# Optimization experiments

Measured on AMD Instinct MI355X. Metric: run time of the kernel, lower is better.

## Reference

```python
import jax, jax.numpy as jnp
import numpy as np

B, C_IN, H, W = 4, 256, 56, 56
REL, OUT, SP, K, PAD = 16, 256, 8, 7, 3
WS = OUT // SP            # 32 attention-weight channels
K2 = K * K                # 49 window taps
EPS = 1e-5


def _unfold(x, k, pad):
    # reflect-pad (SAN pad_mode=1 -> *_refpad kernels) then gather kxk window taps
    # x: [B,C,H,W] -> [B,C,k*k,H,W], tap order row-major (matches torch Unfold)
    xp = jnp.pad(x, ((0, 0), (0, 0), (pad, pad), (pad, pad)), mode='reflect')
    h, w = x.shape[2], x.shape[3]
    return jnp.stack([xp[:, :, i:i + h, j:j + w]
                      for i in range(k) for j in range(k)], axis=2)


def _conv1x1(x, w, b):
    return jnp.einsum('bchw,oc->bohw', x, w) + b[None, :, None, None]


def _bn(x, g, b, m, v):
    # eval-mode BatchNorm2d over channel axis 1, broadcast over trailing dims
    shape = (1, -1) + (1,) * (x.ndim - 2)
    scale = g.reshape(shape) * jax.lax.rsqrt(v.reshape(shape) + EPS)
    return (x - m.reshape(shape)) * scale + b.reshape(shape)


def _forward(x, w1, b1, w2, b2, w3, b3,
             bn1_g, bn1_b, bn1_m, bn1_v, cw1_w,
             bn2_g, bn2_b, bn2_m, bn2_v, cw2_w, cw2_b, pos2_w):
    x1 = _conv1x1(x, w1, b1)          # [B,REL,H,W]  (query)
    x2 = _conv1x1(x, w2, b2)          # [B,REL,H,W]  (key)
    x3 = _conv1x1(x, w3, b3)          # [B,OUT,H,W]  (value)

    # Subtraction2: q_i - k_j for each of K2 window taps -> [B,REL,K2,H,W]
    diff = x1[:, :, None, :, :] - _unfold(x2, K, PAAD) if False else x1[:, :, None, :, :] - _unfold(x2, K, PAD)

    # conv_w: BN -> ReLU -> 1x1 (no bias) -> BN -> ReLU -> 1x1 (bias)
    h = jax.nn.relu(_bn(diff, bn1_g, bn1_b, bn1_m, bn1_v))
    h = jnp.einsum('bckhw,oc->bokhw', h, cw1_w)
    h = jax.nn.relu(_bn(h, bn2_g, bn2_b, bn2_m, bn2_v))
    h = jnp.einsum('bckhw,oc->bokhw', h, cw2_w) + cw2_b[None, :, None, None, None]
    w = jax.nn.softmax(h, axis=2)     # softmax over K2 taps -> [B,WS,K2,H,W]

    # Aggregation: out[b,c,p] = sum_k unfold(x3)[b,c,k,p] * w[b, c//SP, k, p]
    unf3 = _unfold(x3, K, PAD).reshape(B, WS, SP, K2, H, W)
    agg = jnp.einsum('bgskhw,bgkhw->bgshw', unf3, w).reshape(B, OUT, H, W)

    # use_position2: interleave aggregated values with w, grouped 1x1 conv
    xv = agg.reshape(B, SP, WS, H, W).transpose(0, 2, 1, 3, 4)   # [B,WS,SP,H,W]
    xc = jnp.concatenate([xv, w], axis=2)                        # [B,WS,SP+K2,H,W]
    out = jnp.einsum('bgihw,goi->bgohw', xc, pos2_w).reshape(B, OUT, H, W)
    return out


def setup_inputs() -> dict:
    key = jax.random.key(0)
    ks = jax.random.split(key, 20)
    n = lambda k, s, sc=1.0: jax.random.normal(k, s, dtype=jnp.float32) * sc
    u = lambda k, s: jax.random.uniform(k, s, dtype=jnp.float32, minval=0.5, maxval=1.5)
    return {
        'x': n(ks[0], (B, C_IN, H, W)),
        'w1': n(ks[1], (REL, C_IN), 0.05), 'b1': n(ks[2], (REL,), 0.05),
        'w2': n(ks[3], (REL, C_IN), 0.05), 'b2': n(ks[4], (REL,), 0.05),
        'w3': n(ks[5], (OUT, C_IN), 0.05), 'b3': n(ks[6], (OUT,), 0.05),
        'bn1_g': u(ks[7], (REL,)), 'bn1_b': n(ks[8], (REL,), 0.1),
        'bn1_m': n(ks[9], (REL,), 0.1), 'bn1_v': u(ks[10], (REL,)),
        'cw1_w': n(ks[11], (REL, REL), 0.2),
        'bn2_g': u(ks[12], (REL,)), 'bn2_b': n(ks[13], (REL,), 0.1),
        'bn2_m': n(ks[14], (REL,), 0.1), 'bn2_v': u(ks[15], (REL,)),
        'cw2_w': n(ks[16], (WS, REL), 0.2), 'cw2_b': n(ks[17], (WS,), 0.05),
        'pos2_w': n(ks[18], (WS, SP, SP + K2), 0.1),
    }


def reference(x, w1, b1, w2, b2, w3, b3,
              bn1_g, bn1_b, bn1_m, bn1_v, cw1_w,
              bn2_g, bn2_b, bn2_m, bn2_v, cw2_w, cw2_b, pos2_w):
    return _forward(x, w1, b1, w2, b2, w3, b3,
                    bn1_g, bn1_b, bn1_m, bn1_v, cw1_w,
                    bn2_g, bn2_b, bn2_m, bn2_v, cw2_w, cw2_b, pos2_w)
```

## Files before the change

### kernel.cpp

```cpp
#include <hip/hip_runtime.h>

#define HW 56
#define NPIX 3136
#define CIN 256
#define OUTC 256
#define LOG2E 1.4426950408889634f

typedef unsigned short ushort_t;
typedef unsigned int uint_t;
typedef __attribute__((ext_vector_type(8))) short bf16x8;
typedef __attribute__((ext_vector_type(4))) float f32x4;
typedef __attribute__((ext_vector_type(2))) __fp16 half2v;
typedef __attribute__((ext_vector_type(4))) _Float16 f16x4;

__device__ __forceinline__ ushort_t f2b(float f){
  uint_t u = __float_as_uint(f);
  u += 0x7fffu + ((u>>16)&1u);
  return (ushort_t)(u>>16);
}
__device__ __forceinline__ uint_t pkh2(float a, float b){
  union { half2v h; uint_t u; } pk;
  pk.h = __builtin_amdgcn_cvt_pkrtz(a, b);
  return pk.u;
}
__device__ __forceinline__ float h2lo(uint_t u){
  union { ushort_t s; __fp16 h; } c; c.s = (ushort_t)(u & 0xffffu); return (float)c.h;
}
__device__ __forceinline__ float h2hi(uint_t u){
  union { ushort_t s; __fp16 h; } c; c.s = (ushort_t)(u >> 16); return (float)c.h;
}
__device__ __forceinline__ int refl(int v){ v = v<0 ? -v : v; return v>=HW ? 2*HW-2-v : v; }

#define BF_OFF   40960
#define CW1B_OFF 41280
#define CW2B_OFF2 41536
#define CW2B_OFF 42048
#define BNC_OFF  42112
#define P2T_OFF  42176
#define P2H_OFF  56768
#define X1T_OFF  82368
#define X2T_OFF  283072
#define X3_BYTE_OFF 1935104

__global__ void k0_prep(const float* __restrict__ w1, const float* __restrict__ b1,
                        const float* __restrict__ w2, const float* __restrict__ b2,
                        const float* __restrict__ w3, const float* __restrict__ b3,
                        const float* __restrict__ g1, const float* __restrict__ be1,
                        const float* __restrict__ m1, const float* __restrict__ v1,
                        const float* __restrict__ cw1,
                        const float* __restrict__ g2, const float* __restrict__ be2,
                        const float* __restrict__ m2, const float* __restrict__ v2,
                        const float* __restrict__ cw2, const float* __restrict__ cw2b,
                        const float* __restrict__ p2,
                        float* __restrict__ ws)
{
  int idx = blockIdx.x*256 + threadIdx.x;
  if (idx < 81920){
    int j = idx & 7, l = (idx>>3)&63, t2 = idx>>9;
    int nf = t2 % 20, kt = t2 / 20;
    int k = kt*32 + (l>>4)*8 + j;
    int n = nf*16 + (l&15);
    float v = 0.f;
    if (n < 16)       v = w1[n*256 + k];
    else if (n < 32)  v = w2[(n-16)*256 + k];
    else if (n < 288) v = w3[(n-32)*256 + k];
    ((ushort_t*)ws)[idx] = f2b(v);
    return;
  }
  int j = idx - 81920;
  if (j < 288){ ws[BF_OFF+j] = (j<16 ? b1[j] : (j<32 ? b2[j-16] : b3[j-32])); return; }
  j -= 288;
  if (j < 32){ ws[BF_OFF+288+j] = 0.f; return; }
  j -= 32;
  if (j < 128){
    int l = j>>1, q = j&1;
    int n = l & 15, k = ((l>>4)<<2) + 2*q;
    union { __fp16 h[2]; uint_t u; } cv;
    cv.h[0] = (__fp16)cw1[n*16 + k];
    cv.h[1] = (__fp16)cw1[n*16 + k+1];
    ((uint_t*)ws)[CW1B_OFF + j] = cv.u;
    return;
  }
  j -= 128;
  if (j < 256){
    int nf = j>>7, rem = j&127, l = rem>>1, q = rem&1;
    int n = nf*16 + (l & 15), k = ((l>>4)<<2) + 2*q;
    union { __fp16 h[2]; uint_t u; } cv;
    cv.h[0] = (__fp16)(cw2[n*16 + k]   * LOG2E);
    cv.h[1] = (__fp16)(cw2[n*16 + k+1] * LOG2E);
    ((uint_t*)ws)[CW2B_OFF2 + j] = cv.u;
    return;
  }
  j -= 256;
  if (j < 32){ ws[CW2B_OFF+j] = cw2b[j] * LOG2E; return; }
  j -= 32;
  if (j < 64){
    int set = j >> 4, c = j & 15;
    float o;
    if (set == 0){ o = g1[c] * rsqrtf(v1[c] + 1e-5f); }
    else if (set == 1){ float s = g1[c] * rsqrtf(v1[c] + 1e-5f); o = be1[c] - m1[c]*s; }
    else if (set == 2){ o = g2[c] * rsqrtf(v2[c] + 1e-5f); }
    else { float s = g2[c] * rsqrtf(v2[c] + 1e-5f); o = be2[c] - m2[c]*s; }
    ws[BNC_OFF+j] = o;
    return;
  }
  j -= 64;
  if (j < 14592){
    int i = j >> 8, rem = j & 255;
    ws[P2T_OFF + j] = p2[rem*57 + i];
    return;
  }
  j -= 14592;
  if (j < 25600){
    int p = j >> 8, c = j & 255;
    union { __fp16 h[2]; uint_t u; } cv;
    cv.h[0] = (__fp16)p2[c*57 + 8 + 2*p];
    cv.h[1] = (2*p+1 < 49) ? (__fp16)p2[c*57 + 9 + 2*p] : (__fp16)0.f;
    ((uint_t*)ws)[P2H_OFF + j] = cv.u;
    return;
  }
}

__global__ __launch_bounds__(256,4) void k1_proj(const float* __restrict__ x,
                                                 float* __restrict__ ws,
                                                 _Float16* __restrict__ x3h)
{
  __shared__ float xs[CIN*16];
  int t = threadIdx.x;
  int bid = blockIdx.x;
  int b = bid / 196, pp = (bid - b*196)*16;
  int wv = __builtin_amdgcn_readfirstlane(t >> 6);
  int lane = t & 63;

  {
    const float* src = x + (size_t)b*CIN*NPIX + pp;
    int c0 = t >> 2;
    int po = (t & 3) * 4;
    #pragma unroll
    for (int i=0;i<4;i++){
      const float* gp = src + (size_t)(i*64 + c0)*NPIX + po;
      __builtin_amdgcn_global_load_lds(
          (const __attribute__((address_space(1))) void*)gp,
          (__attribute__((address_space(3))) void*)(xs + i*1024 + wv*256),
          16, 0, 0);
    }
  }
  __syncthreads();

  f32x4 acc[5];
  #pragma unroll
  for (int nf=0;nf<5;nf++){
    float bv = ws[BF_OFF + wv*80 + nf*16 + (lane&15)];
    acc[nf] = (f32x4){bv,bv,bv,bv};
  }

  const uint4* bpk = (const uint4*)ws;
  #pragma unroll 1
  for (int kt=0;kt<8;kt++){
    int abase = (kt*32 + ((lane>>4)<<3))*16 + (lane&15);
    union { uint_t u[4]; bf16x8 v; } ahi, alo;
    {
      float f[8];
      #pragma unroll
      for (int j=0;j<8;j++) f[j] = xs[abase + j*16];
      #pragma unroll
      for (int p=0;p<4;p++){
        uint_t u0 = __float_as_uint(f[2*p]), u1 = __float_as_uint(f[2*p+1]);
        uint_t h1 = u1 & 0xffff0000u;
        ahi.u[p] = (u0>>16) | h1;
        float l0 = f[2*p]   - __uint_as_float(u0 & 0xffff0000u);
        float l1 = f[2*p+1] - __uint_as_float(h1);
        alo.u[p] = (__float_as_uint(l0)>>16) | (__float_as_uint(l1) & 0xffff0000u);
      }
    }
    #pragma unroll
    for (int nf=0;nf<5;nf++){
      union { uint4 q; bf16x8 v; } bw;
      bw.q = bpk[(size_t)(kt*20 + wv*5 + nf)*64 + lane];
      acc[nf] = __builtin_amdgcn_mfma_f32_16x16x32_bf16(ahi.v, bw.v, acc[nf], 0,0,0);
      acc[nf] = __builtin_amdgcn_mfma_f32_16x16x32_bf16(alo.v, bw.v, acc[nf], 0,0,0);
    }
  }

  #pragma unroll
  for (int r=0;r<4;r++){
    int sp = pp + ((lane>>4)<<2) + r;
    #pragma unroll
    for (int nf=0;nf<5;nf++){
      int n = wv*80 + nf*16 + (lane&15);
      float val = acc[nf][r];
      if (n < 16){
        ws[X1T_OFF + (size_t)(b*NPIX + sp)*16 + n] = val;
      } else if (n < 32){
        ws[X2T_OFF + (size_t)(b*NPIX + sp)*16 + (n-16)] = val;
      } else if (n < 288){
        x3h[((size_t)b*NPIX + sp)*256 + (n-32)] = (_Float16)val;
      }
    }
  }
}

__global__ __launch_bounds__(256,6) void k2_fused(const float* __restrict__ ws,
                                                  const _Float16* __restrict__ x3h,
                                                  float* __restrict__ out)
{
  __shared__ uint_t lgw[4*864];
  __shared__ __align__(16) ushort_t sA[4*1280];
  __shared__ int    gp_s[4*64];

  int tid = threadIdx.x;
  int bid0 = blockIdx.x;
  int bid = (bid0 & 7)*392 + (bid0 >> 3);
  int b = bid / 784; int rem = bid - b*784;
  int row = rem / 14, xs4 = rem - row*14;
  int wv = __builtin_amdgcn_readfirstlane(tid >> 6);
  int lane = tid & 63;
  int y = row, x = xs4*4 + wv;
  int pix = y*HW + x;

  const float* bnc  = ws + BNC_OFF;
  const float* cw2b = ws + CW2B_OFF;
  uint_t* wvbase = lgw + wv*864;
  ushort_t* sAw = sA + wv*1280;
  int lrow = lane & 15, lk4 = (lane>>4)<<2;

  {
    int k = lane;
    int kk = k < 49 ? k : 48;
    int ki = kk / 7, kj = kk - ki*7;
    int gy = refl(y + ki - 3), gx = refl(x + kj - 3);
    int go = gy*HW + gx;
    gp_s[wv*64 + lane] = go << 9;

    const float*  x1p = ws + X1T_OFF + (size_t)(b*NPIX + pix)*16;
    const float4* x2p = (const float4*)(ws + X2T_OFF + (size_t)(b*NPIX + go)*16);
    float4 v0 = x2p[0], v1 = x2p[1], v2 = x2p[2], v3 = x2p[3];
    float x2v[16] = {v0.x,v0.y,v0.z,v0.w, v1.x,v1.y,v1.z,v1.w,
                     v2.x,v2.y,v2.z,v2.w, v3.x,v3.y,v3.z,v3.w};
    float h1[16];
    #pragma unroll
    for (int c=0;c<16;c++){
      float d = x1p[c] - x2v[c];
      h1[c] = fmaxf(d*bnc[c] + bnc[16+c], 0.f);
    }
    {
      uint2* dst = (uint2*)(sAw + lane*20);
      dst[0] = make_uint2(pkh2(h1[0],h1[1]),  pkh2(h1[2],h1[3]));
      dst[1] = make_uint2(pkh2(h1[4],h1[5]),  pkh2(h1[6],h1[7]));
      dst[2] = make_uint2(pkh2(h1[8],h1[9]),  pkh2(h1[10],h1[11]));
      dst[3] = make_uint2(pkh2(h1[12],h1[13]),pkh2(h1[14],h1[15]));
    }
    union { uint2 u; f16x4 h; } B1, B20, B21;
    B1.u  = ((const uint2*)((const uint_t*)ws + CW1B_OFF))[lane];
    B20.u = ((const uint2*)((const uint_t*)ws + CW2B_OFF2))[lane];
    B21.u = ((const uint2*)((const uint_t*)ws + CW2B_OFF2))[64 + lane];

    float bs2 = bnc[32+lrow], bb2 = bnc[48+lrow];
    #pragma unroll
    for (int m=0;m<4;m++){
      union { uint2 u; f16x4 h; } A;
      A.u = *(const uint2*)(sAw + (m*16+lrow)*20 + lk4);
      f32x4 d = __builtin_amdgcn_mfma_f32_16x16x16f16(A.h, B1.h, (f32x4){0.f,0.f,0.f,0.f}, 0,0,0);
      #pragma unroll
      for (int r=0;r<4;r++){
        float tv = fmaxf(d[r]*bs2 + bb2, 0.f);
        union { __fp16 h; ushort_t s; } th; th.h = (__fp16)tv;
        sAw[(m*16 + lk4 + r)*20 + lrow] = th.s;
      }
    }
    float bg0 = cw2b[lrow], bg1 = cw2b[16+lrow];
    #pragma unroll
    for (int m=0;m<4;m++){
      union { uint2 u; f16x4 h; } A2;
      A2.u = *(const uint2*)(sAw + (m*16+lrow)*20 + lk4);
      f32x4 d0 = __builtin_amdgcn_mfma_f32_16x16x16f16(A2.h, B20.h, (f32x4){bg0,bg0,bg0,bg0}, 0,0,0);
      f32x4 d1 = __builtin_amdgcn_mfma_f32_16x16x16f16(A2.h, B21.h, (f32x4){bg1,bg1,bg1,bg1}, 0,0,0);
      int pq = m*8 + ((lane>>4)<<1);
      uint_t p01 = pkh2(d0[0], d0[1]), p23 = pkh2(d0[2], d0[3]);
      uint_t q01 = pkh2(d1[0], d1[1]), q23 = pkh2(d1[2], d1[3]);
      if (pq < 25){
        wvbase[lrow*27 + pq]      = p01;
        wvbase[(16+lrow)*27 + pq] = q01;
      }
      if (pq+1 < 25){
        wvbase[lrow*27 + pq+1]      = p23;
        wvbase[(16+lrow)*27 + pq+1] = q23;
      }
    }
  }

  {
    int half = lane >> 5, g = lane & 31;
    const uint_t* lgp = wvbase + g*27;
    float e[25];
    float M = -3.0e38f;
    if (half == 0){
      #pragma unroll
      for (int j=0;j<12;j++){
        uint_t u = lgp[j];
        e[2*j]   = h2lo(u);
        e[2*j+1] = h2hi(u);
      }
      e[24] = h2lo(lgp[12]);
      #pragma unroll
      for (int i=0;i<25;i++) M = fmaxf(M, e[i]);
    } else {
      e[0] = h2hi(lgp[12]);
      #pragma unroll
      for (int j=0;j<11;j++){
        uint_t u = lgp[13+j];
        e[1+2*j] = h2lo(u);
        e[2+2*j] = h2hi(u);
      }
      e[23] = h2lo(lgp[24]);
      e[24] = 0.f;
      #pragma unroll
      for (int i=0;i<24;i++) M = fmaxf(M, e[i]);
    }
    M = fmaxf(M, __shfl_xor(M, 32, 64));
    float s = 0.f;
    #pragma unroll
    for (int i=0;i<25;i++){
      if (half == 0 || i < 24){
        e[i] = exp2f(e[i] - M);
        s += e[i];
      }
    }
    s += __shfl_xor(s, 32, 64);
    float inv = 1.f / s;
    #pragma unroll
    for (int i=0;i<25;i++){
      if (half == 0 || i < 24) e[i] *= inv;
    }
    float other = __shfl_xor(half ? e[0] : e[24], 32, 64);
    if (half == 0){
      #pragma unroll
      for (int p=0;p<12;p++) wvbase[p*33 + g] = pkh2(e[2*p], e[2*p+1]);
      wvbase[12*33 + g] = pkh2(e[24], other);
    } else {
      #pragma unroll
      for (int q=0;q<11;q++) wvbase[(13+q)*33 + g] = pkh2(e[1+2*q], e[2+2*q]);
      wvbase[24*33 + g] = pkh2(e[23], 0.f);
    }
  }

  {
    int g_ = lane >> 1;
    int c0 = lane * 4;
    const int* gpp = gp_s + wv*64;
    float a0=0.f,a1=0.f,a2=0.f,a3=0.f;
    const char* xbb = (const char*)(x3h + (size_t)b*NPIX*256) + c0*2;
    #pragma unroll 5
    for (int p=0;p<25;p++){
      uint_t wu = wvbase[p*33 + g_];
      float w0 = h2lo(wu), w1 = h2hi(wu);
      int o0 = gpp[2*p], o1 = gpp[2*p+1];
      union { uint2 u; _Float16 h[4]; } d0, d1;
      d0.u = *(const uint2*)(xbb + o0);
      d1.u = *(const uint2*)(xbb + o1);
      a0 += w0*(float)d0.h[0] + w1*(float)d1.h[0];
      a1 += w0*(float)d0.h[1] + w1*(float)d1.h[1];
      a2 += w0*(float)d0.h[2] + w1*(float)d1.h[2];
      a3 += w0*(float)d0.h[3] + w1*(float)d1.h[3];
    }
    float* agw = (float*)(sA + wv*1280);
    *(float4*)&agw[c0] = make_float4(a0,a1,a2,a3);
  }
  __syncthreads();

  {
    int c = tid, g4 = c >> 3;
    const float* P2 = ws + P2T_OFF;
    const uint_t* P2H = (const uint_t*)ws + P2H_OFF;
    const float* ag0 = (const float*)(sA + 0*1280);
    const float* ag1 = (const float*)(sA + 1*1280);
    const float* ag2 = (const float*)(sA + 2*1280);
    const float* ag3 = (const float*)(sA + 3*1280);
    float r0=0.f, r1=0.f, r2=0.f, r3=0.f;
    #pragma unroll
    for (int i=0;i<8;i++){
      float pv = P2[i*256 + c];
      r0 += ag0[i*32 + g4] * pv;
      r1 += ag1[i*32 + g4] * pv;
      r2 += ag2[i*32 + g4] * pv;
      r3 += ag3[i*32 + g4] * pv;
    }
    #pragma unroll 5
    for (int p=0;p<25;p++){
      union { uint_t u; half2v h; } ph; ph.u = P2H[p*256 + c];
      union { uint_t u; half2v h; } w0, w1, w2, w3;
      w0.u = lgw[0*864 + p*33 + g4];
      w1.u = lgw[1*864 + p*33 + g4];
      w2.u = lgw[2*864 + p*33 + g4];
      w3.u = lgw[3*864 + p*33 + g4];
      r0 = __builtin_amdgcn_fdot2(w0.h, ph.h, r0, false);
      r1 = __builtin_amdgcn_fdot2(w1.h, ph.h, r1, false);
      r2 = __builtin_amdgcn_fdot2(w2.h, ph.h, r2, false);
      r3 = __builtin_amdgcn_fdot2(w3.h, ph.h, r3, false);
    }
    int pix0 = y*HW + xs4*4;
    *(float4*)(out + ((size_t)(b*256 + c))*NPIX + pix0) = make_float4(r0,r1,r2,r3);
  }
}

extern "C" void kernel_launch(void* const* d_in, const int* in_sizes, int n_in,
                              void* d_out, int out_size, void* d_ws, size_t ws_size,
                              hipStream_t stream) {
  const float* x    = (const float*)d_in[0];
  const float* w1   = (const float*)d_in[1];
  const float* b1   = (const float*)d_in[2];
  const float* w2   = (const float*)d_in[3];
  const float* b2   = (const float*)d_in[4];
  const float* w3   = (const float*)d_in[5];
  const float* b3   = (const float*)d_in[6];
  const float* g1   = (const float*)d_in[7];
  const float* be1  = (const float*)d_in[8];
  const float* m1   = (const float*)d_in[9];
  const float* v1   = (const float*)d_in[10];
  const float* cw1  = (const float*)d_in[11];
  const float* g2   = (const float*)d_in[12];
  const float* be2  = (const float*)d_in[13];
  const float* m2   = (const float*)d_in[14];
  const float* v2   = (const float*)d_in[15];
  const float* cw2  = (const float*)d_in[16];
  const float* cw2b = (const float*)d_in[17];
  const float* p2   = (const float*)d_in[18];

  float* wsf = (float*)d_ws;
  _Float16* x3h = (_Float16*)((char*)d_ws + X3_BYTE_OFF);
  float* o = (float*)d_out;

  k0_prep<<<481, 256, 0, stream>>>(w1,b1,w2,b2,w3,b3,g1,be1,m1,v1,cw1,g2,be2,m2,v2,cw2,cw2b,p2,wsf);
  k1_proj<<<784, 256, 0, stream>>>(x, wsf, x3h);
  k2_fused<<<3136, 256, 0, stream>>>(wsf, x3h, o);
}
```

Before: 57.56 us.

## Defer softmax normalization and interleave per-wave weights in shared memory for vector reads

Softmax no longer multiplies the 49 probabilities by 1/sum. The reciprocal is stored in shared memory and applied after aggregation and after the position dot-product. Softmax weights and aggregated values are written into new transposed shared buffers, interleaved across the four waves, so the final stage reads all four pixels with one 16-byte load instead of four scalar loads. This adds a block barrier before softmax, a larger shared footprint, and lowers launch-bounds occupancy from 6 to 4 blocks. It also keeps unnormalized exponentials in fp16, which changes precision.

```diff
diff --git a/kernel.cpp b/kernel.cpp
--- a/kernel.cpp
+++ b/kernel.cpp
@@ -28,6 +28,10 @@
 }
 __device__ __forceinline__ float h2hi(uint_t u){
   union { ushort_t s; __fp16 h; } c; c.s = (ushort_t)(u >> 16); return (float)c.h;
+}
+__device__ __forceinline__ float fdot2u(uint_t w, uint_t v, float acc){
+  union { uint_t u; half2v h; } a, b; a.u = w; b.u = v;
+  return __builtin_amdgcn_fdot2(a.h, b.h, acc, false);
 }
 __device__ __forceinline__ int refl(int v){ v = v<0 ? -v : v; return v>=HW ? 2*HW-2-v : v; }
 
@@ -200,11 +204,12 @@
   }
 }
 
-__global__ __launch_bounds__(256,6) void k2_fused(const float* __restrict__ ws,
+__global__ __launch_bounds__(256,4) void k2_fused(const float* __restrict__ ws,
                                                   const _Float16* __restrict__ x3h,
                                                   float* __restrict__ out)
 {
   __shared__ uint_t lgw[4*864];
+  __shared__ __align__(16) uint_t wT[25*132];
   __shared__ __align__(16) ushort_t sA[4*1280];
   __shared__ int    gp_s[4*64];
 
@@ -222,6 +227,8 @@
   const float* cw2b = ws + CW2B_OFF;
   uint_t* wvbase = lgw + wv*864;
   ushort_t* sAw = sA + wv*1280;
+  float* agsT = (float*)sA;
+  float* invsL = (float*)sA + 1056;
   int lrow = lane & 15, lk4 = (lane>>4)<<2;
 
   {
@@ -289,6 +296,8 @@
     }
   }
 
+  __syncthreads();
+
   {
     int half = lane >> 5, g = lane & 31;
     const uint_t* lgp = wvbase + g*27;
@@ -327,20 +336,16 @@
       }
     }
     s += __shfl_xor(s, 32, 64);
-    float inv = 1.f / s;
-    #pragma unroll
-    for (int i=0;i<25;i++){
-      if (half == 0 || i < 24) e[i] *= inv;
-    }
+    if (half == 0) invsL[wv*32 + g] = 1.f / s;
     float other = __shfl_xor(half ? e[0] : e[24], 32, 64);
     if (half == 0){
       #pragma unroll
-      for (int p=0;p<12;p++) wvbase[p*33 + g] = pkh2(e[2*p], e[2*p+1]);
-      wvbase[12*33 + g] = pkh2(e[24], other);
+      for (int p=0;p<12;p++) wT[p*132 + g*4 + wv] = pkh2(e[2*p], e[2*p+1]);
+      wT[12*132 + g*4 + wv] = pkh2(e[24], other);
     } else {
       #pragma unroll
-      for (int q=0;q<11;q++) wvbase[(13+q)*33 + g] = pkh2(e[1+2*q], e[2+2*q]);
-      wvbase[24*33 + g] = pkh2(e[23], 0.f);
+      for (int q=0;q<11;q++) wT[(13+q)*132 + g*4 + wv] = pkh2(e[1+2*q], e[2+2*q]);
+      wT[24*132 + g*4 + wv] = pkh2(e[23], 0.f);
     }
   }
 
@@ -352,7 +357,7 @@
     const char* xbb = (const char*)(x3h + (size_t)b*NPIX*256) + c0*2;
     #pragma unroll 5
     for (int p=0;p<25;p++){
-      uint_t wu = wvbase[p*33 + g_];
+      uint_t wu = wT[p*132 + g_*4 + wv];
       float w0 = h2lo(wu), w1 = h2hi(wu);
       int o0 = gpp[2*p], o1 = gpp[2*p+1];
       union { uint2 u; _Float16 h[4]; } d0, d1;
@@ -363,8 +368,11 @@
       a2 += w0*(float)d0.h[2] + w1*(float)d1.h[2];
       a3 += w0*(float)d0.h[3] + w1*(float)d1.h[3];
     }
-    float* agw = (float*)(sA + wv*1280);
-    *(float4*)&agw[c0] = make_float4(a0,a1,a2,a3);
+    float inv = invsL[wv*32 + g_];
+    a0 *= inv; a1 *= inv; a2 *= inv; a3 *= inv;
+    int ii = lane >> 3, gb = (lane & 7) * 4;
+    float* dst = agsT + ii*132 + gb*4 + wv;
+    dst[0] = a0; dst[4] = a1; dst[8] = a2; dst[12] = a3;
   }
   __syncthreads();
 
@@ -372,32 +380,27 @@
     int c = tid, g4 = c >> 3;
     const float* P2 = ws + P2T_OFF;
     const uint_t* P2H = (const uint_t*)ws + P2H_OFF;
-    const float* ag0 = (const float*)(sA + 0*1280);
-    const float* ag1 = (const float*)(sA + 1*1280);
-    const float* ag2 = (const float*)(sA + 2*1280);
-    const float* ag3 = (const float*)(sA + 3*1280);
     float r0=0.f, r1=0.f, r2=0.f, r3=0.f;
     #pragma unroll
     for (int i=0;i<8;i++){
+      f32x4 av = *(const f32x4*)(agsT + i*132 + g4*4);
       float pv = P2[i*256 + c];
-      r0 += ag0[i*32 + g4] * pv;
-      r1 += ag1[i*32 + g4] * pv;
-      r2 += ag2[i*32 + g4] * pv;
-      r3 += ag3[i*32 + g4] * pv;
-    }
+      r0 += av[0]*pv; r1 += av[1]*pv; r2 += av[2]*pv; r3 += av[3]*pv;
+    }
+    float t0=0.f, t1=0.f, t2=0.f, t3=0.f;
     #pragma unroll 5
     for (int p=0;p<25;p++){
-      union { uint_t u; half2v h; } ph; ph.u = P2H[p*256 + c];
-      union { uint_t u; half2v h; } w0, w1, w2, w3;
-      w0.u = lgw[0*864 + p*33 + g4];
-      w1.u = lgw[1*864 + p*33 + g4];
-      w2.u = lgw[2*864 + p*33 + g4];
-      w3.u = lgw[3*864 + p*33 + g4];
-      r0 = __builtin_amdgcn_fdot2(w0.h, ph.h, r0, false);
-      r1 = __builtin_amdgcn_fdot2(w1.h, ph.h, r1, false);
-      r2 = __builtin_amdgcn_fdot2(w2.h, ph.h, r2, false);
-      r3 = __builtin_amdgcn_fdot2(w3.h, ph.h, r3, false);
-    }
+      uint4 wq = *(const uint4*)(wT + p*132 + g4*4);
+      uint_t ph = P2H[p*256 + c];
+      t0 = fdot2u(wq.x, ph, t0);
+      t1 = fdot2u(wq.y, ph, t1);
+      t2 = fdot2u(wq.z, ph, t2);
+      t3 = fdot2u(wq.w, ph, t3);
+    }
+    r0 += t0 * invsL[0*32 + g4];
+    r1 += t1 * invsL[1*32 + g4];
+    r2 += t2 * invsL[2*32 + g4];
+    r3 += t3 * invsL[3*32 + g4];
     int pix0 = y*HW + xs4*4;
     *(float4*)(out + ((size_t)(b*256 + c))*NPIX + pix0) = make_float4(r0,r1,r2,r3);
   }
```

Measured after the change: 59.65 us. 1.04x slower.
